# Kernel optimization log

Measured on AMD Instinct MI355X. Metric: run time of the kernel, lower is better.

## Reference

```python
import jax, jax.numpy as jnp
import numpy as np

B, T, E, H = 8, 1024, 768, 12  # batch, num_tokens, embed_dim (=dk=dv), num_heads


def setup_inputs() -> dict:
    key = jax.random.key(0)
    ks = jax.random.split(key, 5)
    return {
        "x": jax.random.normal(ks[0], (B, T, E), dtype=jnp.float32),
        "WQ": jax.random.normal(ks[1], (H, E, E), dtype=jnp.float32),
        "WK": jax.random.normal(ks[2], (H, E, E), dtype=jnp.float32),
        "WV": jax.random.normal(ks[3], (H, E, E), dtype=jnp.float32),
        "WO": jax.random.normal(ks[4], (H * E, E), dtype=jnp.float32),
    }


def reference(x, WQ, WK, WV, WO):
    b, t, e = x.shape
    h = WQ.shape[0]
    dk = WQ.shape[2]
    dv = WV.shape[2]
    # Batched QKV projections for all heads at once: (h, b, t, d)
    Q = jnp.einsum('bte,hek->hbtk', x, WQ)
    K = jnp.einsum('bte,hek->hbtk', x, WK)
    V = jnp.einsum('bte,hev->hbtv', x, WV)
    # Faithful quirk: original does K.view(b, e, t) -- a row-major RESHAPE,
    # not a transpose (valid because dk == e).
    K_rs = K.reshape(h, b, e, t)
    scores = jnp.matmul(Q, K_rs)  # (h, b, t, t)
    # Faithful quirks: scale by sqrt(num_tokens) (K.size(1) == t), and
    # Softmax(1) normalizes over the QUERY axis (axis 1 of (b,t,t) -> axis -2).
    A = jax.nn.softmax(scores / jnp.sqrt(jnp.asarray(t, scores.dtype)), axis=-2)
    Z = jnp.matmul(A, V)  # (h, b, t, dv)
    # Original: Z[bb] has layout (h, t, dv); reshape(t, h*dv) flat in row-major.
    Zc = jnp.transpose(Z, (1, 0, 2, 3)).reshape(b, h, t, dv)
    Zc = Zc.reshape(b, h * t * dv).reshape(b, t, h * dv)  # row-major flat of (h,t,dv)
    return jnp.matmul(Zc, WO)  # (b, t, e)
```

## Files before the change

kernel.cpp:

```cpp
#include <hip/hip_runtime.h>


typedef __bf16 bf16x8 __attribute__((ext_vector_type(8)));
typedef float  f32x4  __attribute__((ext_vector_type(4)));
typedef unsigned short u16;
typedef u16 u16x2 __attribute__((ext_vector_type(2)));
typedef u16 u16x4 __attribute__((ext_vector_type(4)));
typedef unsigned int u32;

#define RC 16

__device__ __forceinline__ float bf2f(u16 u) {
    union { u32 i; float f; } x; x.i = ((u32)u) << 16; return x.f;
}
__device__ __forceinline__ u16 f2bf(float f) {
    __bf16 h = (__bf16)f; union { __bf16 b; u16 u; } x; x.b = h; return x.u;
}
__device__ __forceinline__ void split2(float v, u16& h, u16& l) {
    h = f2bf(v); l = f2bf(v - bf2f(h));
}

__device__ __forceinline__ void gl16(const void* g, void* l) {
    __builtin_amdgcn_global_load_lds(
        (const __attribute__((address_space(1))) u32*)g,
        (__attribute__((address_space(3))) u32*)l, 16, 0, 0);
}

template<int WIN>
__device__ __forceinline__ void core(
    const u16* __restrict__ Ah, const u16* __restrict__ Al,
    const u16* __restrict__ Bh, const u16* __restrict__ Bl,
    float* __restrict__ C, u16* __restrict__ Ch, u16* __restrict__ Cl,
    int K, int lda, int ldb, int ldc,
    long long aShift, long long aHi, const u16* __restrict__ zp,
    int mClip, int mode, int mtile, int kChunk, int kChunks, int n0)
{
    __shared__ u16 Ahs[4096], Als[4096], Bhs[4096], Bls[4096];

    const int tid = threadIdx.x, lane = tid & 63, w = tid >> 6;
    const int m0 = mtile * 128;
    const int wm = (w & 1) << 6, wn = (w >> 1) << 6;
    const int lr = lane & 15, lq = lane >> 4;
    const int rs = (lr >> 1) & 3;
    const int fro = (lq ^ rs) << 4;

    const int srow = (w << 4) + (lane >> 2);
    const int kk = (((lane & 3) ^ ((srow >> 1) & 3)) << 3);
    const int lds0 = (w << 10), lds1 = lds0 + 4096;

    f32x4 acc[4][4] = {};
    const int kLen = K / kChunks;
    const int kBeg = kChunk * kLen, kEnd = kBeg + kLen;

    auto stage = [&](int k0) {
        long long o1 = (long long)(m0 + srow) * lda + k0 + kk;
        long long o2 = o1 + (long long)64 * lda;
        const u16 *p1h = Ah + o1, *p1l = Al + o1;
        const u16 *p2h = Ah + o2, *p2l = Al + o2;
        if constexpr (WIN) {
            long long a1 = o1 + aShift, a2 = o2 + aShift;
            bool v1 = (a1 >= 0) && (a1 < aHi);
            bool v2 = (a2 >= 0) && (a2 < aHi);
            p1h = v1 ? Ah + a1 : zp;  p1l = v1 ? Al + a1 : zp;
            p2h = v2 ? Ah + a2 : zp;  p2l = v2 ? Al + a2 : zp;
        }
        gl16(p1h, (char*)Ahs + lds0);  gl16(p2h, (char*)Ahs + lds1);
        gl16(p1l, (char*)Als + lds0);  gl16(p2l, (char*)Als + lds1);
        long long b1 = (long long)(n0 + srow) * ldb + k0 + kk;
        long long b2 = b1 + (long long)64 * ldb;
        gl16(Bh + b1, (char*)Bhs + lds0);  gl16(Bh + b2, (char*)Bhs + lds1);
        gl16(Bl + b1, (char*)Bls + lds0);  gl16(Bl + b2, (char*)Bls + lds1);
    };

    for (int k0 = kBeg; k0 < kEnd; k0 += 32) {
        stage(k0);
        __syncthreads();

        bf16x8 a_h[4], a_l[4];
#pragma unroll
        for (int mi = 0; mi < 4; ++mi) {
            int off = ((wm + (mi << 4) + lr) << 6) + fro;
            a_h[mi] = *(const bf16x8*)((char*)Ahs + off);
            a_l[mi] = *(const bf16x8*)((char*)Als + off);
        }
#pragma unroll
        for (int ni = 0; ni < 4; ++ni) {
            int off = ((wn + (ni << 4) + lr) << 6) + fro;
            bf16x8 b_h = *(const bf16x8*)((char*)Bhs + off);
            bf16x8 b_l = *(const bf16x8*)((char*)Bls + off);
#pragma unroll
            for (int mi = 0; mi < 4; ++mi) {
                acc[mi][ni] = __builtin_amdgcn_mfma_f32_16x16x32_bf16(a_h[mi], b_h, acc[mi][ni], 0, 0, 0);
                acc[mi][ni] = __builtin_amdgcn_mfma_f32_16x16x32_bf16(a_l[mi], b_h, acc[mi][ni], 0, 0, 0);
                acc[mi][ni] = __builtin_amdgcn_mfma_f32_16x16x32_bf16(a_h[mi], b_l, acc[mi][ni], 0, 0, 0);
            }
        }
        __syncthreads();
    }

#pragma unroll
    for (int mi = 0; mi < 4; ++mi)
#pragma unroll
        for (int r = 0; r < 4; ++r) {
            int row = m0 + wm + (mi << 4) + (lq << 2) + r;
            if (row < mClip) {
#pragma unroll
                for (int ni = 0; ni < 4; ++ni) {
                    long long off = (long long)row * ldc + n0 + wn + (ni << 4) + lr;
                    float v = acc[mi][ni][r];
                    if (mode == 2)      atomicAdd(&C[off], v);
                    else if (mode == 1) { u16 hh, ll; split2(v, hh, ll); Ch[off] = hh; Cl[off] = ll; }
                    else                C[off] = v;
                }
            }
        }
}

__global__ __launch_bounds__(256, 4)
void g_qkv(const u16* __restrict__ Xh, const u16* __restrict__ Xl,
           const u16* __restrict__ Wth, const u16* __restrict__ Wtl,
           u16* __restrict__ Qh, u16* __restrict__ Ql,
           u16* __restrict__ Kh, u16* __restrict__ Kl,
           u16* __restrict__ Vh, u16* __restrict__ Vl)
{
    const long long EE = 768LL * 768;
    int z  = blockIdx.x % 3;
    int n0 = (blockIdx.x / 3) * 128;
    const u16* bh = Wth + (long long)z * EE;
    const u16* bl = Wtl + (long long)z * EE;
    u16* ch = (z == 0) ? Qh : (z == 1) ? Kh : Vh;
    u16* cl = (z == 0) ? Ql : (z == 1) ? Kl : Vl;
    core<0>(Xh, Xl, bh, bl, nullptr, ch, cl, 768, 768, 768, 768,
            0, 0, nullptr, 1 << 30, 1, blockIdx.y, 0, 1, n0);
}

__global__ __launch_bounds__(256, 4)
void g_bt(const u16* __restrict__ Ah, const u16* __restrict__ Al,
          const u16* __restrict__ Bh, const u16* __restrict__ Bl,
          u16* __restrict__ Ch, u16* __restrict__ Cl,
          int K, int lda, int ldb, int ldc,
          long long sA, long long sB, long long sC)
{
    long long z = blockIdx.z;
    core<0>(Ah + z * sA, Al + z * sA, Bh + z * sB, Bl + z * sB,
            nullptr, Ch + z * sC, Cl + z * sC,
            K, lda, ldb, ldc, 0, 0, nullptr, 1 << 30, 1,
            blockIdx.y, 0, 1, blockIdx.x * 128);
}

__global__ __launch_bounds__(256, 4)
void g_fin(const u16* __restrict__ Zh, const u16* __restrict__ Zl,
           const u16* __restrict__ WOth, const u16* __restrict__ WOtl,
           float* __restrict__ C, const u16* __restrict__ zp,
           long long aShift, int mClip, int kChunks)
{
    const long long TE_ = 786432;
    long long z = blockIdx.z;
    core<1>(Zh + z * TE_, Zl + z * TE_, WOth, WOtl, C + z * TE_,
            nullptr, nullptr, 9216, 9216, 9216, 768,
            aShift, TE_, zp, mClip, 2, 0, blockIdx.y, kChunks, blockIdx.x * 128);
}

__global__ __launch_bounds__(256)
void t_hl(const u16* __restrict__ ih, const u16* __restrict__ il,
          u16* __restrict__ oh, u16* __restrict__ ol, int R, int C)
{
    long long zo = (long long)blockIdx.z * R * C;
    __shared__ u16 L[64][34];
    const int t = threadIdx.x, tx = t & 31, ty = t >> 5;
    const int r0 = blockIdx.y * 32, c0 = blockIdx.x * 64;
    const int orow = t >> 2;

    const u16* iv[2] = { ih + zo, il + zo };
    u16* ov[2] = { oh + zo, ol + zo };
#pragma unroll
    for (int p = 0; p < 2; ++p) {
        const u16* in = iv[p];  u16* out = ov[p];
#pragma unroll
        for (int i = 0; i < 4; ++i) {
            u16x2 v = *(const u16x2*)&in[(long long)(r0 + ty + 8 * i) * C + c0 + tx * 2];
            L[tx * 2][ty + 8 * i] = v[0];
            L[tx * 2 + 1][ty + 8 * i] = v[1];
        }
        __syncthreads();
#pragma unroll
        for (int i = 0; i < 4; ++i) {
            int j = (t & 3) * 4 + i;
            u16x2 wv;
            wv[0] = L[orow][j * 2];
            wv[1] = L[orow][j * 2 + 1];
            *(u16x2*)&out[(long long)(c0 + orow) * R + r0 + j * 2] = wv;
        }
        __syncthreads();
    }
}

__global__ void k_split(const float* __restrict__ s, u16* __restrict__ h,
                        u16* __restrict__ l, long long n)
{
    long long i = ((long long)blockIdx.x * blockDim.x + threadIdx.x) * 4;
    long long stride = (long long)gridDim.x * blockDim.x * 4;
    for (; i < n; i += stride) {
        float4 v = *(const float4*)(s + i);
        u16x4 hh, ll;
        u16 h0, l0, h1, l1, h2, l2, h3, l3;
        split2(v.x, h0, l0); split2(v.y, h1, l1);
        split2(v.z, h2, l2); split2(v.w, h3, l3);
        hh[0] = h0; hh[1] = h1; hh[2] = h2; hh[3] = h3;
        ll[0] = l0; ll[1] = l1; ll[2] = l2; ll[3] = l3;
        *(u16x4*)(h + i) = hh;
        *(u16x4*)(l + i) = ll;
    }
}

__global__ void k_tsplit(const float* __restrict__ s, u16* __restrict__ dh,
                         u16* __restrict__ dl, int Ks, int Ns)
{
    __shared__ float t[32][33];
    int tx = threadIdx.x & 31, ty = threadIdx.x >> 5;
    int kb = blockIdx.y << 5, nb_ = blockIdx.x << 5;
#pragma unroll
    for (int i = 0; i < 4; ++i)
        t[ty + 8 * i][tx] = s[(long long)(kb + ty + 8 * i) * Ns + nb_ + tx];
    __syncthreads();
#pragma unroll
    for (int i = 0; i < 4; ++i) {
        float v = t[tx][ty + 8 * i];
        long long o = (long long)(nb_ + ty + 8 * i) * Ks + kb + tx;
        u16 hh, ll; split2(v, hh, ll);
        dh[o] = hh; dl[o] = ll;
    }
}

__global__ void k_tsplit3(const float* __restrict__ s0, const float* __restrict__ s1,
                          const float* __restrict__ s2,
                          u16* __restrict__ dh, u16* __restrict__ dl)
{
    const int E = 768; const long long EE = (long long)E * E;
    const float* s = (blockIdx.z == 0) ? s0 : (blockIdx.z == 1) ? s1 : s2;
    u16* h = dh + blockIdx.z * EE;
    u16* l = dl + blockIdx.z * EE;
    __shared__ float t[32][33];
    int tx = threadIdx.x & 31, ty = threadIdx.x >> 5;
    int kb = blockIdx.y << 5, nb_ = blockIdx.x << 5;
#pragma unroll
    for (int i = 0; i < 4; ++i)
        t[ty + 8 * i][tx] = s[(long long)(kb + ty + 8 * i) * E + nb_ + tx];
    __syncthreads();
#pragma unroll
    for (int i = 0; i < 4; ++i) {
        float v = t[tx][ty + 8 * i];
        long long o = (long long)(nb_ + ty + 8 * i) * E + kb + tx;
        u16 hh, ll; split2(v, hh, ll);
        h[o] = hh; l[o] = ll;
    }
}

__global__ __launch_bounds__(256)
void sm_part(const u16* __restrict__ Sh, const u16* __restrict__ Sl,
             float2* __restrict__ part, int T, float scale)
{
    const int lane = threadIdx.x & 63, seg = threadIdx.x >> 6;
    const int j0 = blockIdx.x * 256 + lane * 4;
    const long long base = (long long)blockIdx.z * T * T;
    const int rpc = T / RC, rps = rpc / 4;
    const int r0 = blockIdx.y * rpc + seg * rps;

    float m[4] = {-3.4e38f, -3.4e38f, -3.4e38f, -3.4e38f};
    float s[4] = {0.f, 0.f, 0.f, 0.f};
    for (int r = 0; r < rps; ++r) {
        long long o = base + (long long)(r0 + r) * T + j0;
        u16x4 vh = *(const u16x4*)(Sh + o);
        u16x4 vl = *(const u16x4*)(Sl + o);
#pragma unroll
        for (int c = 0; c < 4; ++c) {
            float v = (bf2f(vh[c]) + bf2f(vl[c])) * scale;
            float mn = fmaxf(m[c], v);
            s[c] = s[c] * __expf(m[c] - mn) + __expf(v - mn);
            m[c] = mn;
        }
    }
    __shared__ float4 smm[4][64], sss[4][64];
    smm[seg][lane] = make_float4(m[0], m[1], m[2], m[3]);
    sss[seg][lane] = make_float4(s[0], s[1], s[2], s[3]);
    __syncthreads();
    if (seg == 0) {
#pragma unroll
        for (int q = 1; q < 4; ++q) {
            float4 mq4 = smm[q][lane], sq4 = sss[q][lane];
            float mq[4] = {mq4.x, mq4.y, mq4.z, mq4.w};
            float sq[4] = {sq4.x, sq4.y, sq4.z, sq4.w};
#pragma unroll
            for (int c = 0; c < 4; ++c) {
                float mn = fmaxf(m[c], mq[c]);
                s[c] = s[c] * __expf(m[c] - mn) + sq[c] * __expf(mq[c] - mn);
                m[c] = mn;
            }
        }
        long long pb = ((long long)blockIdx.z * RC + blockIdx.y) * T + j0;
#pragma unroll
        for (int c = 0; c < 4; ++c)
            part[pb + c] = make_float2(m[c], s[c]);
    }
}

__global__ __launch_bounds__(256)
void sm_fin2(const float2* __restrict__ part, float2* __restrict__ fin, int T)
{
    int j = blockIdx.x * 256 + threadIdx.x;
    long long pb = (long long)blockIdx.y * RC * T + j;
    float mt = -3.4e38f, st = 0.f;
#pragma unroll
    for (int q = 0; q < RC; ++q) {
        float2 p = part[pb + (long long)q * T];
        float mn = fmaxf(mt, p.x);
        st = st * __expf(mt - mn) + p.y * __expf(p.x - mn);
        mt = mn;
    }
    fin[(long long)blockIdx.y * T + j] = make_float2(mt, 1.f / st);
}

__global__ __launch_bounds__(256)
void sm_norm(u16* __restrict__ Sh, u16* __restrict__ Sl,
             const float2* __restrict__ fin, int T, float scale)
{
    const int lane = threadIdx.x & 63, seg = threadIdx.x >> 6;
    const int j0 = blockIdx.x * 256 + lane * 4;
    const long long base = (long long)blockIdx.z * T * T;
    const int rpc = T / RC, rps = rpc / 4;
    const int r0 = blockIdx.y * rpc + seg * rps;
    float mt[4], inv[4];
#pragma unroll
    for (int c = 0; c < 4; ++c) {
        float2 f = fin[(long long)blockIdx.z * T + j0 + c];
        mt[c] = f.x; inv[c] = f.y;
    }
    for (int r = 0; r < rps; ++r) {
        long long o = base + (long long)(r0 + r) * T + j0;
        u16x4 vh = *(const u16x4*)(Sh + o);
        u16x4 vl = *(const u16x4*)(Sl + o);
        u16x4 oh, ol;
#pragma unroll
        for (int c = 0; c < 4; ++c) {
            float v = (bf2f(vh[c]) + bf2f(vl[c])) * scale;
            float p = __expf(v - mt[c]) * inv[c];
            u16 hh, ll; split2(p, hh, ll);
            oh[c] = hh; ol[c] = ll;
        }
        *(u16x4*)(Sh + o) = oh;
        *(u16x4*)(Sl + o) = ol;
    }
}

extern "C" void kernel_launch(void* const* d_in, const int* in_sizes, int n_in,
                              void* d_out, int out_size, void* d_ws, size_t ws_size,
                              hipStream_t stream)
{
    const float* x  = (const float*)d_in[0];
    const float* WQ = (const float*)d_in[1];
    const float* WK = (const float*)d_in[2];
    const float* WV = (const float*)d_in[3];
    const float* WO = (const float*)d_in[4];
    float* out = (float*)d_out;

    const int B = 8, T = 1024, E = 768, H = 12;
    const long long TE = (long long)T * E;
    const long long TT = (long long)T * T;
    const long long HE = (long long)H * E;
    const long long EE = (long long)E * E;

    char* p = (char*)d_ws;
    u16* Xh   = (u16*)p; p += (size_t)B * TE * 2;
    u16* Xl   = (u16*)p; p += (size_t)B * TE * 2;
    u16* WOth = (u16*)p; p += (size_t)E * HE * 2;
    u16* WOtl = (u16*)p; p += (size_t)E * HE * 2;
    u16* Wth  = (u16*)p; p += (size_t)3 * EE * 2;
    u16* Wtl  = (u16*)p; p += (size_t)3 * EE * 2;
    u16* zp   = (u16*)p; p += 4096;
    float2* part = (float2*)p; p += (size_t)B * RC * T * sizeof(float2);
    float2* finb = (float2*)p; p += (size_t)B * T * sizeof(float2);
    size_t used = (size_t)(p - (char*)d_ws);
    size_t slice = (size_t)(8 * TE + 2 * TT) * 2;
    int NC = (int)((ws_size - used) / slice);
    if (NC < 1) NC = 1;
    if (NC > B) NC = B;
    u16* Qh  = (u16*)p; p += (size_t)NC * TE * 2;
    u16* Ql  = (u16*)p; p += (size_t)NC * TE * 2;
    u16* Kh  = (u16*)p; p += (size_t)NC * TE * 2;
    u16* Kl  = (u16*)p; p += (size_t)NC * TE * 2;
    u16* Vh  = (u16*)p; p += (size_t)NC * TE * 2;
    u16* Vl  = (u16*)p; p += (size_t)NC * TE * 2;
    u16* Kth = (u16*)p; p += (size_t)NC * TE * 2;
    u16* Ktl = (u16*)p; p += (size_t)NC * TE * 2;
    u16* Sh  = (u16*)p; p += (size_t)NC * TT * 2;
    u16* Sl  = (u16*)p; p += (size_t)NC * TT * 2;
    u16* Zh = Qh;
    u16* Zl = Ql;
    u16* Vth = Kh;
    u16* Vtl = Kl;

    hipMemsetAsync(out, 0, (size_t)B * TE * sizeof(float), stream);
    hipMemsetAsync(zp, 0, 4096, stream);

    dim3 blk(256);

    k_split<<<2048, blk, 0, stream>>>(x, Xh, Xl, (long long)B * TE);
    k_tsplit<<<dim3(E / 32, (int)HE / 32), blk, 0, stream>>>(WO, WOth, WOtl, (int)HE, E);

    for (int h = 0; h < H; ++h) {
        const int i_lo = (int)(((long long)h * TE) / HE);
        const long long aShift = (long long)i_lo * HE - (long long)h * TE;

        k_tsplit3<<<dim3(24, 24, 3), blk, 0, stream>>>(
            WQ + (size_t)h * EE, WK + (size_t)h * EE, WV + (size_t)h * EE, Wth, Wtl);

        for (int b0 = 0; b0 < B; b0 += NC) {
            const int nb = (B - b0 < NC) ? (B - b0) : NC;

            g_qkv<<<dim3(18, nb * T / 128), blk, 0, stream>>>(
                Xh + (size_t)b0 * TE, Xl + (size_t)b0 * TE, Wth, Wtl,
                Qh, Ql, Kh, Kl, Vh, Vl);

            t_hl<<<dim3(16, 24, nb), blk, 0, stream>>>(Kh, Kl, Kth, Ktl, 768, 1024);
            t_hl<<<dim3(12, 32, nb), blk, 0, stream>>>(Vh, Vl, Vth, Vtl, 1024, 768);

            g_bt<<<dim3(8, 8, nb), blk, 0, stream>>>(
                Qh, Ql, Kth, Ktl, Sh, Sl, 768, 768, 768, 1024, TE, TE, TT);

            sm_part<<<dim3(T / 256, RC, nb), blk, 0, stream>>>(Sh, Sl, part, T, 0.03125f);
            sm_fin2<<<dim3(T / 256, nb), blk, 0, stream>>>(part, finb, T);
            sm_norm<<<dim3(T / 256, RC, nb), blk, 0, stream>>>(Sh, Sl, finb, T, 0.03125f);

            g_bt<<<dim3(6, 8, nb), blk, 0, stream>>>(
                Sh, Sl, Vth, Vtl, Zh, Zl, 1024, 1024, 1024, 768, TT, TE, TE);

            g_fin<<<dim3(6, 24, nb), blk, 0, stream>>>(
                Zh, Zl, WOth, WOtl,
                out + (size_t)b0 * TE + (size_t)i_lo * E, zp,
                aShift, T - i_lo, 24);
        }
    }
}
```

Baseline: 4.340 ms.

## Buffer all-head Z per batch chunk and run one output projection GEMM

Swaps the loop nesting to batch-outer, head-inner. When workspace allows, each head's attention output Z is written into a buffer covering all 12 heads, and a single GEMM against WO runs per batch chunk with two K-chunks. This replaces 12 per-head clipped output-projection launches with fewer, larger GEMM launches. In exchange it re-splits the per-head weights once per batch chunk instead of once per head, and it needs extra workspace.

```diff
diff --git a/kernel.cpp b/kernel.cpp
--- a/kernel.cpp
+++ b/kernel.cpp
@@ -146,6 +146,20 @@
             nullptr, Ch + z * sC, Cl + z * sC,
             K, lda, ldb, ldc, 0, 0, nullptr, 1 << 30, 1,
             blockIdx.y, 0, 1, blockIdx.x * 128);
+}
+
+__global__ __launch_bounds__(256, 4)
+void g_out(const u16* __restrict__ Zh, const u16* __restrict__ Zl,
+           const u16* __restrict__ WOth, const u16* __restrict__ WOtl,
+           float* __restrict__ C, int kChunks)
+{
+    const long long ZB = 12LL * 786432;
+    long long z = blockIdx.z;
+    int mtile = blockIdx.y / kChunks;
+    int kc    = blockIdx.y % kChunks;
+    core<0>(Zh + z * ZB, Zl + z * ZB, WOth, WOtl, C + z * 786432LL,
+            nullptr, nullptr, 9216, 9216, 9216, 768,
+            0, 0, nullptr, 1 << 30, 2, mtile, kc, kChunks, blockIdx.x * 128);
 }
 
 __global__ __launch_bounds__(256, 4)
@@ -380,10 +394,16 @@
     float2* part = (float2*)p; p += (size_t)B * RC * T * sizeof(float2);
     float2* finb = (float2*)p; p += (size_t)B * T * sizeof(float2);
     size_t used = (size_t)(p - (char*)d_ws);
-    size_t slice = (size_t)(8 * TE + 2 * TT) * 2;
+
+    size_t slice  = (size_t)(8 * TE + 2 * TT) * 2;
+    size_t zslice = (size_t)12 * TE * 4;
     int NC = (int)((ws_size - used) / slice);
     if (NC < 1) NC = 1;
     if (NC > B) NC = B;
+    int NC_A = (int)((ws_size - used) / (slice + zslice));
+    if (NC_A > B) NC_A = B;
+    const bool tierA = (NC_A >= NC);
+
     u16* Qh  = (u16*)p; p += (size_t)NC * TE * 2;
     u16* Ql  = (u16*)p; p += (size_t)NC * TE * 2;
     u16* Kh  = (u16*)p; p += (size_t)NC * TE * 2;
@@ -394,6 +414,8 @@
     u16* Ktl = (u16*)p; p += (size_t)NC * TE * 2;
     u16* Sh  = (u16*)p; p += (size_t)NC * TT * 2;
     u16* Sl  = (u16*)p; p += (size_t)NC * TT * 2;
+    u16* Zallh = (u16*)p; if (tierA) p += (size_t)NC * 12 * TE * 2;
+    u16* Zalll = (u16*)p;
     u16* Zh = Qh;
     u16* Zl = Ql;
     u16* Vth = Kh;
@@ -407,15 +429,12 @@
     k_split<<<2048, blk, 0, stream>>>(x, Xh, Xl, (long long)B * TE);
     k_tsplit<<<dim3(E / 32, (int)HE / 32), blk, 0, stream>>>(WO, WOth, WOtl, (int)HE, E);
 
-    for (int h = 0; h < H; ++h) {
-        const int i_lo = (int)(((long long)h * TE) / HE);
-        const long long aShift = (long long)i_lo * HE - (long long)h * TE;
-
-        k_tsplit3<<<dim3(24, 24, 3), blk, 0, stream>>>(
-            WQ + (size_t)h * EE, WK + (size_t)h * EE, WV + (size_t)h * EE, Wth, Wtl);
-
-        for (int b0 = 0; b0 < B; b0 += NC) {
-            const int nb = (B - b0 < NC) ? (B - b0) : NC;
+    for (int b0 = 0; b0 < B; b0 += NC) {
+        const int nb = (B - b0 < NC) ? (B - b0) : NC;
+
+        for (int h = 0; h < H; ++h) {
+            k_tsplit3<<<dim3(24, 24, 3), blk, 0, stream>>>(
+                WQ + (size_t)h * EE, WK + (size_t)h * EE, WV + (size_t)h * EE, Wth, Wtl);
 
             g_qkv<<<dim3(18, nb * T / 128), blk, 0, stream>>>(
                 Xh + (size_t)b0 * TE, Xl + (size_t)b0 * TE, Wth, Wtl,
@@ -431,13 +450,26 @@
             sm_fin2<<<dim3(T / 256, nb), blk, 0, stream>>>(part, finb, T);
             sm_norm<<<dim3(T / 256, RC, nb), blk, 0, stream>>>(Sh, Sl, finb, T, 0.03125f);
 
-            g_bt<<<dim3(6, 8, nb), blk, 0, stream>>>(
-                Sh, Sl, Vth, Vtl, Zh, Zl, 1024, 1024, 1024, 768, TT, TE, TE);
-
-            g_fin<<<dim3(6, 24, nb), blk, 0, stream>>>(
-                Zh, Zl, WOth, WOtl,
-                out + (size_t)b0 * TE + (size_t)i_lo * E, zp,
-                aShift, T - i_lo, 24);
-        }
-    }
-}
+            if (tierA) {
+                g_bt<<<dim3(6, 8, nb), blk, 0, stream>>>(
+                    Sh, Sl, Vth, Vtl,
+                    Zallh + (size_t)h * TE, Zalll + (size_t)h * TE,
+                    1024, 1024, 1024, 768, TT, TE, 12 * TE);
+            } else {
+                const int i_lo = (int)(((long long)h * TE) / HE);
+                const long long aShift = (long long)i_lo * HE - (long long)h * TE;
+                g_bt<<<dim3(6, 8, nb), blk, 0, stream>>>(
+                    Sh, Sl, Vth, Vtl, Zh, Zl, 1024, 1024, 1024, 768, TT, TE, TE);
+                g_fin<<<dim3(6, 24, nb), blk, 0, stream>>>(
+                    Zh, Zl, WOth, WOtl,
+                    out + (size_t)b0 * TE + (size_t)i_lo * E, zp,
+                    aShift, T - i_lo, 24);
+            }
+        }
+
+        if (tierA) {
+            g_out<<<dim3(6, 8 * 2, nb), blk, 0, stream>>>(
+                Zallh, Zalll, WOth, WOtl, out + (size_t)b0 * TE, 2);
+        }
+    }
+}
```

New measurement: 4.305 ms. About the same (-0.8%).
